# Optimization experiments

Hardware: AMD Instinct MI355X
Metric: run time of the kernel (lower is better)

Reference implementation:

```python
import jax, jax.numpy as jnp
import numpy as np

B, D_IN, D_H = 4096, 1024, 2048


def setup_inputs() -> dict:
    key = jax.random.key(0)
    ks = jax.random.split(key, 16)
    s_in = 1.0 / np.sqrt(D_IN)
    s_h = 1.0 / np.sqrt(D_H)
    inp = {
        "x": jax.random.normal(ks[0], (B, D_IN), jnp.float32),
        "h_prev": jax.random.normal(ks[1], (B, D_H), jnp.float32),
        "c_prev": jax.random.normal(ks[2], (B, D_H), jnp.float32),
        "n_prev": jax.random.uniform(ks[3], (B, D_H), jnp.float32) + 0.5,
        # input-gate weights [D_H, D_IN] (torch Linear layout) + biases
        "Wz": jax.random.uniform(ks[4], (D_H, D_IN), jnp.float32, -s_in, s_in),
        "Wi": jax.random.uniform(ks[5], (D_H, D_IN), jnp.float32, -s_in, s_in),
        "Wf": jax.random.uniform(ks[6], (D_H, D_IN), jnp.float32, -s_in, s_in),
        "Wo": jax.random.uniform(ks[7], (D_H, D_IN), jnp.float32, -s_in, s_in),
        "bz": jax.random.uniform(ks[8], (D_H,), jnp.float32, -s_in, s_in),
        "bi": jax.random.uniform(ks[9], (D_H,), jnp.float32, -s_in, s_in),
        "bf": jax.random.uniform(ks[10], (D_H,), jnp.float32, -s_in, s_in),
        "bo": jax.random.uniform(ks[11], (D_H,), jnp.float32, -s_in, s_in),
        # recurrent weights [D_H, D_H], bias-free
        "Rz": jax.random.uniform(ks[12], (D_H, D_H), jnp.float32, -s_h, s_h),
        "Ri": jax.random.uniform(ks[13], (D_H, D_H), jnp.float32, -s_h, s_h),
        "Rf": jax.random.uniform(ks[14], (D_H, D_H), jnp.float32, -s_h, s_h),
        "Ro": jax.random.uniform(ks[15], (D_H, D_H), jnp.float32, -s_h, s_h),
    }
    return inp


def reference(x, h_prev, c_prev, n_prev,
              Wz, Wi, Wf, Wo, bz, bi, bf, bo,
              Rz, Ri, Rf, Ro):
    # Fuse the 4 input GEMMs and 4 recurrent GEMMs into two batched contractions.
    Wcat = jnp.concatenate([Wz, Wi, Wf, Wo], axis=0)      # [4H, D_IN]
    Rcat = jnp.concatenate([Rz, Ri, Rf, Ro], axis=0)      # [4H, H]
    bcat = jnp.concatenate([bz, bi, bf, bo], axis=0)      # [4H]
    pre = x @ Wcat.T + h_prev @ Rcat.T + bcat              # [B, 4H]
    az, ai, af, ao = jnp.split(pre, 4, axis=1)
    z = jnp.tanh(az)
    i = jnp.exp(ai)
    f = jnp.exp(af)
    o = jax.nn.sigmoid(ao)
    c = f * c_prev + i * z
    n = f * n_prev + i
    h = o * (c / n)
    return h
```

## Files before the change

kernel.cpp:

```cpp
#include <hip/hip_runtime.h>
#include <hip/hip_fp16.h>

#define B_SZ  4096
#define DIN   1024
#define DH    2048
#define K_TOT 3072
#define N_TOT 8192

#define BM 128
#define BN 128
#define BK 64

typedef _Float16 half8 __attribute__((ext_vector_type(8)));
typedef float   float4v __attribute__((ext_vector_type(4)));

__device__ __forceinline__ void load_lds16(const void* g, void* l) {
    __builtin_amdgcn_global_load_lds(
        (const __attribute__((address_space(1))) void*)g,
        (__attribute__((address_space(3))) void*)l,
        16, 0, 0);
}

#define A_BLOCKS ((B_SZ * K_TOT / 8) / 256)
#define W_BLOCKS ((N_TOT * K_TOT / 8) / 256)

__global__ __launch_bounds__(256) void cast_all_kernel(
        const float* __restrict__ x, const float* __restrict__ h,
        const float* __restrict__ Wz, const float* __restrict__ Wi,
        const float* __restrict__ Wf, const float* __restrict__ Wo,
        const float* __restrict__ Rz, const float* __restrict__ Ri,
        const float* __restrict__ Rf, const float* __restrict__ Ro,
        _Float16* __restrict__ A, _Float16* __restrict__ Wb) {
    const float* src;
    _Float16* dst;
    if (blockIdx.x < A_BLOCKS) {
        int idx = (blockIdx.x * 256 + threadIdx.x) * 8;
        int b = idx / K_TOT;
        int c = idx - b * K_TOT;
        src = (c < DIN) ? (x + (size_t)b * DIN + c) : (h + (size_t)b * DH + (c - DIN));
        dst = A + idx;
    } else {
        int idx = ((blockIdx.x - A_BLOCKS) * 256 + threadIdx.x) * 8;
        int n = idx / K_TOT;
        int c = idx - n * K_TOT;
        int t = n & 127;
        int g = (t >> 4) & 3;
        int j = ((n >> 7) << 5) + ((t >> 6) << 4) + (t & 15);
        const float* W = (g == 0) ? Wz : (g == 1) ? Wi : (g == 2) ? Wf : Wo;
        const float* R = (g == 0) ? Rz : (g == 1) ? Ri : (g == 2) ? Rf : Ro;
        src = (c < DIN) ? (W + (size_t)j * DIN + c) : (R + (size_t)j * DH + (c - DIN));
        dst = Wb + idx;
    }
    float4 v0 = *reinterpret_cast<const float4*>(src);
    float4 v1 = *reinterpret_cast<const float4*>(src + 4);
    half8 o;
    o[0] = (_Float16)v0.x; o[1] = (_Float16)v0.y;
    o[2] = (_Float16)v0.z; o[3] = (_Float16)v0.w;
    o[4] = (_Float16)v1.x; o[5] = (_Float16)v1.y;
    o[6] = (_Float16)v1.z; o[7] = (_Float16)v1.w;
    *reinterpret_cast<half8*>(dst) = o;
}

__global__ __launch_bounds__(256) void slstm_gemm_kernel(
        const _Float16* __restrict__ A, const _Float16* __restrict__ Wb,
        const float* __restrict__ c_prev, const float* __restrict__ n_prev,
        const float* __restrict__ bz, const float* __restrict__ bi,
        const float* __restrict__ bf, const float* __restrict__ bo,
        float* __restrict__ Hout) {
    __shared__ __align__(16) _Float16 As[BM * BK];
    __shared__ __align__(16) _Float16 Bs[BN * BK];

    const int ntile = blockIdx.x;
    const int mtile = blockIdx.y;
    const int tid  = threadIdx.x;
    const int wv   = tid >> 6;
    const int wm   = wv >> 1;
    const int wn   = wv & 1;
    const int l    = tid & 63;
    const int quad = l >> 4;
    const int l16  = l & 15;

    const int m0 = mtile * BM;
    const int n0 = ntile * BN;

    float4v acc[4][4];
#pragma unroll
    for (int i = 0; i < 4; i++)
#pragma unroll
        for (int j = 0; j < 4; j++) acc[i][j] = (float4v){0.f, 0.f, 0.f, 0.f};

    const int lrow  = l >> 3;
    const int skoff = (((l & 7) ^ (lrow & 7)) * 8);

    const int r0 = wv * 32 + lrow;
    const _Float16* Ag0 = A  + (size_t)(m0 + r0)      * K_TOT + skoff;
    const _Float16* Ag1 = A  + (size_t)(m0 + r0 + 8)  * K_TOT + skoff;
    const _Float16* Ag2 = A  + (size_t)(m0 + r0 + 16) * K_TOT + skoff;
    const _Float16* Ag3 = A  + (size_t)(m0 + r0 + 24) * K_TOT + skoff;
    const _Float16* Bg0 = Wb + (size_t)(n0 + r0)      * K_TOT + skoff;
    const _Float16* Bg1 = Wb + (size_t)(n0 + r0 + 8)  * K_TOT + skoff;
    const _Float16* Bg2 = Wb + (size_t)(n0 + r0 + 16) * K_TOT + skoff;
    const _Float16* Bg3 = Wb + (size_t)(n0 + r0 + 24) * K_TOT + skoff;

    _Float16* AsL0 = As + (wv * 4 + 0) * 512;
    _Float16* AsL1 = As + (wv * 4 + 1) * 512;
    _Float16* AsL2 = As + (wv * 4 + 2) * 512;
    _Float16* AsL3 = As + (wv * 4 + 3) * 512;
    _Float16* BsL0 = Bs + (wv * 4 + 0) * 512;
    _Float16* BsL1 = Bs + (wv * 4 + 1) * 512;
    _Float16* BsL2 = Bs + (wv * 4 + 2) * 512;
    _Float16* BsL3 = Bs + (wv * 4 + 3) * 512;

    const int kq0 = (((0 * 4 + quad) ^ (l16 & 7)) * 8);
    const int kq1 = (((1 * 4 + quad) ^ (l16 & 7)) * 8);

    for (int kt = 0; kt < K_TOT; kt += BK) {
        load_lds16(Ag0 + kt, AsL0);
        load_lds16(Ag1 + kt, AsL1);
        load_lds16(Ag2 + kt, AsL2);
        load_lds16(Ag3 + kt, AsL3);
        load_lds16(Bg0 + kt, BsL0);
        load_lds16(Bg1 + kt, BsL1);
        load_lds16(Bg2 + kt, BsL2);
        load_lds16(Bg3 + kt, BsL3);
        __syncthreads();

#pragma unroll
        for (int kp = 0; kp < 2; kp++) {
            const int kq = kp ? kq1 : kq0;
            half8 afr[4], bfr[4];
#pragma unroll
            for (int mf = 0; mf < 4; mf++)
                afr[mf] = *reinterpret_cast<const half8*>(As + (wm * 64 + mf * 16 + l16) * BK + kq);
#pragma unroll
            for (int nf = 0; nf < 4; nf++)
                bfr[nf] = *reinterpret_cast<const half8*>(Bs + (wn * 64 + nf * 16 + l16) * BK + kq);

#pragma unroll
            for (int mf = 0; mf < 4; mf++)
#pragma unroll
                for (int nf = 0; nf < 4; nf++)
                    acc[mf][nf] = __builtin_amdgcn_mfma_f32_16x16x32_f16(afr[mf], bfr[nf], acc[mf][nf], 0, 0, 0);
        }
        __syncthreads();
    }

    const int j = ntile * 32 + wn * 16 + l16;
    const float bzv = bz[j], biv = bi[j], bfv = bf[j], bov = bo[j];
#pragma unroll
    for (int mf = 0; mf < 4; mf++) {
#pragma unroll
        for (int r = 0; r < 4; r++) {
            const int row = m0 + wm * 64 + mf * 16 + quad * 4 + r;
            const size_t off = (size_t)row * DH + j;
            const float az  = acc[mf][0][r] + bzv;
            const float ai  = acc[mf][1][r] + biv;
            const float af_ = acc[mf][2][r] + bfv;
            const float ao  = acc[mf][3][r] + bov;
            const float ax = fabsf(az);
            const float e2 = __expf(-2.0f * ax);
            float tz = __fdividef(1.0f - e2, 1.0f + e2);
            tz = (az >= 0.0f) ? tz : -tz;
            const float iv = __expf(ai);
            const float fv = __expf(af_);
            const float ov = __fdividef(1.0f, 1.0f + __expf(-ao));
            const float cc = fv * c_prev[off] + iv * tz;
            const float nn = fv * n_prev[off] + iv;
            Hout[off] = ov * __fdividef(cc, nn);
        }
    }
}

extern "C" void kernel_launch(void* const* d_in, const int* in_sizes, int n_in,
                              void* d_out, int out_size, void* d_ws, size_t ws_size,
                              hipStream_t stream) {
    const float* x      = (const float*)d_in[0];
    const float* h_prev = (const float*)d_in[1];
    const float* c_prev = (const float*)d_in[2];
    const float* n_prev = (const float*)d_in[3];
    const float* Wz = (const float*)d_in[4];
    const float* Wi = (const float*)d_in[5];
    const float* Wf = (const float*)d_in[6];
    const float* Wo = (const float*)d_in[7];
    const float* bz = (const float*)d_in[8];
    const float* bi = (const float*)d_in[9];
    const float* bf = (const float*)d_in[10];
    const float* bo = (const float*)d_in[11];
    const float* Rz = (const float*)d_in[12];
    const float* Ri = (const float*)d_in[13];
    const float* Rf = (const float*)d_in[14];
    const float* Ro = (const float*)d_in[15];

    _Float16* A  = (_Float16*)d_ws;
    _Float16* Wb = A + (size_t)B_SZ * K_TOT;

    cast_all_kernel<<<A_BLOCKS + W_BLOCKS, 256, 0, stream>>>(
        x, h_prev, Wz, Wi, Wf, Wo, Rz, Ri, Rf, Ro, A, Wb);

    dim3 grid(N_TOT / BN, B_SZ / BM);
    slstm_gemm_kernel<<<grid, 256, 0, stream>>>(
        A, Wb, c_prev, n_prev, bz, bi, bf, bo, (float*)d_out);
}
```

Baseline: 453.7 us.

## Use 256x256 tiles with double-buffered LDS, staged prefetch and block swizzle

Enlarges the GEMM tile to 256x256 with 8 waves and double-buffers LDS so global-to-LDS loads for the next K step overlap MFMA work on the current one. The main loop is split into four phases, each with its own barrier and s_setprio around the MFMA bursts. A block-index swizzle is added for L2 reuse, and the weight interleave layout is changed so each wave's columns match the new tile. In exchange it uses more registers (32 accumulators per lane) and 128KB of LDS per block, and the hand-counted vmcnt waits could be fragile.

```diff
diff --git a/kernel.cpp b/kernel.cpp
--- a/kernel.cpp
+++ b/kernel.cpp
@@ -7,9 +7,10 @@
 #define K_TOT 3072
 #define N_TOT 8192
 
-#define BM 128
-#define BN 128
+#define BM 256
+#define BN 256
 #define BK 64
+#define NK (K_TOT / BK)
 
 typedef _Float16 half8 __attribute__((ext_vector_type(8)));
 typedef float   float4v __attribute__((ext_vector_type(4)));
@@ -43,9 +44,8 @@
         int idx = ((blockIdx.x - A_BLOCKS) * 256 + threadIdx.x) * 8;
         int n = idx / K_TOT;
         int c = idx - n * K_TOT;
-        int t = n & 127;
-        int g = (t >> 4) & 3;
-        int j = ((n >> 7) << 5) + ((t >> 6) << 4) + (t & 15);
+        int g = (n >> 6) & 3;
+        int j = ((n >> 8) << 6) | (n & 63);
         const float* W = (g == 0) ? Wz : (g == 1) ? Wi : (g == 2) ? Wf : Wo;
         const float* R = (g == 0) ? Rz : (g == 1) ? Ri : (g == 2) ? Rf : Ro;
         src = (c < DIN) ? (W + (size_t)j * DIN + c) : (R + (size_t)j * DH + (c - DIN));
@@ -61,97 +61,131 @@
     *reinterpret_cast<half8*>(dst) = o;
 }
 
-__global__ __launch_bounds__(256) void slstm_gemm_kernel(
+__global__ __launch_bounds__(512, 2) void slstm_gemm_kernel(
         const _Float16* __restrict__ A, const _Float16* __restrict__ Wb,
         const float* __restrict__ c_prev, const float* __restrict__ n_prev,
         const float* __restrict__ bz, const float* __restrict__ bi,
         const float* __restrict__ bf, const float* __restrict__ bo,
         float* __restrict__ Hout) {
-    __shared__ __align__(16) _Float16 As[BM * BK];
-    __shared__ __align__(16) _Float16 Bs[BN * BK];
-
-    const int ntile = blockIdx.x;
-    const int mtile = blockIdx.y;
+    __shared__ __align__(16) _Float16 As[2][BM * BK];
+    __shared__ __align__(16) _Float16 Bs[2][BN * BK];
+
+    const int bid   = blockIdx.x;
+    const int swz   = (bid & 7) * 64 + (bid >> 3);
+    const int ntile = swz & 31;
+    const int mtile = swz >> 5;
+    const int m0 = mtile * BM;
+    const int n0 = ntile * BN;
+
     const int tid  = threadIdx.x;
     const int wv   = tid >> 6;
-    const int wm   = wv >> 1;
-    const int wn   = wv & 1;
+    const int wm   = wv >> 2;
+    const int wn   = wv & 3;
     const int l    = tid & 63;
     const int quad = l >> 4;
     const int l16  = l & 15;
 
-    const int m0 = mtile * BM;
-    const int n0 = ntile * BN;
-
-    float4v acc[4][4];
-#pragma unroll
-    for (int i = 0; i < 4; i++)
+    float4v acc[8][4];
+#pragma unroll
+    for (int i = 0; i < 8; i++)
 #pragma unroll
         for (int j = 0; j < 4; j++) acc[i][j] = (float4v){0.f, 0.f, 0.f, 0.f};
 
     const int lrow  = l >> 3;
-    const int skoff = (((l & 7) ^ (lrow & 7)) * 8);
-
-    const int r0 = wv * 32 + lrow;
-    const _Float16* Ag0 = A  + (size_t)(m0 + r0)      * K_TOT + skoff;
-    const _Float16* Ag1 = A  + (size_t)(m0 + r0 + 8)  * K_TOT + skoff;
-    const _Float16* Ag2 = A  + (size_t)(m0 + r0 + 16) * K_TOT + skoff;
-    const _Float16* Ag3 = A  + (size_t)(m0 + r0 + 24) * K_TOT + skoff;
-    const _Float16* Bg0 = Wb + (size_t)(n0 + r0)      * K_TOT + skoff;
-    const _Float16* Bg1 = Wb + (size_t)(n0 + r0 + 8)  * K_TOT + skoff;
-    const _Float16* Bg2 = Wb + (size_t)(n0 + r0 + 16) * K_TOT + skoff;
-    const _Float16* Bg3 = Wb + (size_t)(n0 + r0 + 24) * K_TOT + skoff;
-
-    _Float16* AsL0 = As + (wv * 4 + 0) * 512;
-    _Float16* AsL1 = As + (wv * 4 + 1) * 512;
-    _Float16* AsL2 = As + (wv * 4 + 2) * 512;
-    _Float16* AsL3 = As + (wv * 4 + 3) * 512;
-    _Float16* BsL0 = Bs + (wv * 4 + 0) * 512;
-    _Float16* BsL1 = Bs + (wv * 4 + 1) * 512;
-    _Float16* BsL2 = Bs + (wv * 4 + 2) * 512;
-    _Float16* BsL3 = Bs + (wv * 4 + 3) * 512;
-
-    const int kq0 = (((0 * 4 + quad) ^ (l16 & 7)) * 8);
-    const int kq1 = (((1 * 4 + quad) ^ (l16 & 7)) * 8);
-
-    for (int kt = 0; kt < K_TOT; kt += BK) {
-        load_lds16(Ag0 + kt, AsL0);
-        load_lds16(Ag1 + kt, AsL1);
-        load_lds16(Ag2 + kt, AsL2);
-        load_lds16(Ag3 + kt, AsL3);
-        load_lds16(Bg0 + kt, BsL0);
-        load_lds16(Bg1 + kt, BsL1);
-        load_lds16(Bg2 + kt, BsL2);
-        load_lds16(Bg3 + kt, BsL3);
-        __syncthreads();
-
-#pragma unroll
-        for (int kp = 0; kp < 2; kp++) {
-            const int kq = kp ? kq1 : kq0;
-            half8 afr[4], bfr[4];
-#pragma unroll
-            for (int mf = 0; mf < 4; mf++)
-                afr[mf] = *reinterpret_cast<const half8*>(As + (wm * 64 + mf * 16 + l16) * BK + kq);
-#pragma unroll
-            for (int nf = 0; nf < 4; nf++)
-                bfr[nf] = *reinterpret_cast<const half8*>(Bs + (wn * 64 + nf * 16 + l16) * BK + kq);
-
-#pragma unroll
-            for (int mf = 0; mf < 4; mf++)
-#pragma unroll
-                for (int nf = 0; nf < 4; nf++)
-                    acc[mf][nf] = __builtin_amdgcn_mfma_f32_16x16x32_f16(afr[mf], bfr[nf], acc[mf][nf], 0, 0, 0);
-        }
-        __syncthreads();
-    }
-
-    const int j = ntile * 32 + wn * 16 + l16;
+    const int skoff = ((l & 7) ^ lrow) * 8;
+    const _Float16* Ag = A  + (size_t)(m0 + wv * 16 + lrow) * K_TOT + skoff;
+    const _Float16* Bg = Wb + (size_t)(n0 + wv * 16 + lrow) * K_TOT + skoff;
+    const int ldsA = wv * 1024;
+
+#define STAGE_A(h, nb, kk) do { \
+    load_lds16(Ag + (size_t)(h) * 128 * K_TOT + (kk),        &As[nb][(h) * 8192 + ldsA]); \
+    load_lds16(Ag + ((size_t)(h) * 128 + 8) * K_TOT + (kk),  &As[nb][(h) * 8192 + ldsA + 512]); } while (0)
+#define STAGE_B(h, nb, kk) do { \
+    load_lds16(Bg + (size_t)(h) * 128 * K_TOT + (kk),        &Bs[nb][(h) * 8192 + ldsA]); \
+    load_lds16(Bg + ((size_t)(h) * 128 + 8) * K_TOT + (kk),  &Bs[nb][(h) * 8192 + ldsA + 512]); } while (0)
+
+    const int aRowBase = wm * 16 + l16;
+    const int bColBase = wn * 16 + l16;
+    const int sl0 = ((0 + quad) ^ (l16 & 7)) * 8;
+    const int sl1 = ((4 + quad) ^ (l16 & 7)) * 8;
+
+    half8 afr[4][2], bfr0[2][2], bfr1[2][2];
+
+#define LOAD_A(MB) \
+    _Pragma("unroll") \
+    for (int mf = 0; mf < 4; ++mf) { \
+        const _Float16* p = Ac + (size_t)(aRowBase + ((MB) + mf) * 32) * BK; \
+        afr[mf][0] = *reinterpret_cast<const half8*>(p + sl0); \
+        afr[mf][1] = *reinterpret_cast<const half8*>(p + sl1); \
+    }
+#define LOAD_B(DST, NB) \
+    _Pragma("unroll") \
+    for (int nf = 0; nf < 2; ++nf) { \
+        const _Float16* p = Bc + (size_t)(bColBase + ((NB) + nf) * 64) * BK; \
+        DST[nf][0] = *reinterpret_cast<const half8*>(p + sl0); \
+        DST[nf][1] = *reinterpret_cast<const half8*>(p + sl1); \
+    }
+#define MFMA16(MB, NB, BF) \
+    _Pragma("unroll") \
+    for (int kp = 0; kp < 2; ++kp) \
+    _Pragma("unroll") \
+    for (int mf = 0; mf < 4; ++mf) \
+    _Pragma("unroll") \
+    for (int nf = 0; nf < 2; ++nf) \
+        acc[(MB) + mf][(NB) + nf] = __builtin_amdgcn_mfma_f32_16x16x32_f16( \
+            afr[mf][kp], BF[nf][kp], acc[(MB) + mf][(NB) + nf], 0, 0, 0);
+
+    STAGE_A(0, 0, 0);
+    STAGE_B(0, 0, 0);
+    STAGE_B(1, 0, 0);
+    STAGE_A(1, 0, 0);
+
+    for (int kt = 0; kt < NK; ++kt) {
+        const int cur = kt & 1;
+        const int nxt = cur ^ 1;
+        const int kk  = (kt + 1 < NK) ? (kt + 1) * BK : 0;
+        const _Float16* Ac = &As[cur][0];
+        const _Float16* Bc = &Bs[cur][0];
+
+        asm volatile("s_waitcnt vmcnt(4)" ::: "memory");
+        __builtin_amdgcn_s_barrier();
+        LOAD_A(0);
+        LOAD_B(bfr0, 0);
+        STAGE_A(0, nxt, kk);
+        __builtin_amdgcn_s_setprio(1);
+        MFMA16(0, 0, bfr0);
+        __builtin_amdgcn_s_setprio(0);
+
+        asm volatile("s_waitcnt vmcnt(4)" ::: "memory");
+        __builtin_amdgcn_s_barrier();
+        LOAD_B(bfr1, 2);
+        STAGE_B(0, nxt, kk);
+        __builtin_amdgcn_s_setprio(1);
+        MFMA16(0, 2, bfr1);
+        __builtin_amdgcn_s_setprio(0);
+
+        asm volatile("s_waitcnt vmcnt(4)" ::: "memory");
+        __builtin_amdgcn_s_barrier();
+        LOAD_A(4);
+        STAGE_B(1, nxt, kk);
+        __builtin_amdgcn_s_setprio(1);
+        MFMA16(4, 2, bfr1);
+        __builtin_amdgcn_s_setprio(0);
+
+        __builtin_amdgcn_s_barrier();
+        STAGE_A(1, nxt, kk);
+        __builtin_amdgcn_s_setprio(1);
+        MFMA16(4, 0, bfr0);
+        __builtin_amdgcn_s_setprio(0);
+    }
+
+    const int j = ntile * 64 + wn * 16 + l16;
     const float bzv = bz[j], biv = bi[j], bfv = bf[j], bov = bo[j];
 #pragma unroll
-    for (int mf = 0; mf < 4; mf++) {
-#pragma unroll
-        for (int r = 0; r < 4; r++) {
-            const int row = m0 + wm * 64 + mf * 16 + quad * 4 + r;
+    for (int mf = 0; mf < 8; ++mf) {
+#pragma unroll
+        for (int r = 0; r < 4; ++r) {
+            const int row = m0 + mf * 32 + wm * 16 + quad * 4 + r;
             const size_t off = (size_t)row * DH + j;
             const float az  = acc[mf][0][r] + bzv;
             const float ai  = acc[mf][1][r] + biv;
@@ -169,6 +203,11 @@
             Hout[off] = ov * __fdividef(cc, nn);
         }
     }
+#undef STAGE_A
+#undef STAGE_B
+#undef LOAD_A
+#undef LOAD_B
+#undef MFMA16
 }
 
 extern "C" void kernel_launch(void* const* d_in, const int* in_sizes, int n_in,
@@ -197,7 +236,7 @@
     cast_all_kernel<<<A_BLOCKS + W_BLOCKS, 256, 0, stream>>>(
         x, h_prev, Wz, Wi, Wf, Wo, Rz, Ri, Rf, Ro, A, Wb);
 
-    dim3 grid(N_TOT / BN, B_SZ / BM);
-    slstm_gemm_kernel<<<grid, 256, 0, stream>>>(
+    dim3 grid(N_TOT / BN * (B_SZ / BM));
+    slstm_gemm_kernel<<<grid, 512, 0, stream>>>(
         A, Wb, c_prev, n_prev, bz, bi, bf, bo, (float*)d_out);
 }
```

New measurement: 441.1 us. 2.8% less time.
